# Optimization experiments

Hardware: AMD Instinct MI355X
Metric: run time of the kernel (lower is better)

The kernel has to match this reference:

```python
import jax, jax.numpy as jnp
import numpy as np

IN_F, OUT_F = 768, 2304
E, R = 8, 16            # num adapters, lora rank
ALPHA = 32
SCALING = ALPHA / R
GATE_DIM = 64


def setup_inputs() -> dict:
    key = jax.random.key(0)
    ks = jax.random.split(key, 8)
    B, S = 8, 2048
    x = jax.random.normal(ks[0], (B, S, IN_F), dtype=jnp.float32)
    z = jax.random.normal(ks[1], (B, GATE_DIM), dtype=jnp.float32)
    # frozen linear (nn.Linear weight layout [out, in])
    W = jax.random.normal(ks[2], (OUT_F, IN_F), dtype=jnp.float32) * 0.02
    b = jax.random.normal(ks[3], (OUT_F,), dtype=jnp.float32) * 0.02
    # stacked LoRA adapters: A [E, r, in], B [E, out, r]
    A = jax.random.normal(ks[4], (E, R, IN_F), dtype=jnp.float32) * (1.0 / np.sqrt(IN_F))
    Bm = jax.random.normal(ks[5], (E, OUT_F, R), dtype=jnp.float32) * 0.02
    # spectral gate: linear + softmax over experts
    Wg = jax.random.normal(ks[6], (E, GATE_DIM), dtype=jnp.float32) * 0.1
    bg = jax.random.normal(ks[7], (E,), dtype=jnp.float32) * 0.1
    return {"x": x, "z": z, "W": W, "b": b, "A": A, "Bm": Bm, "Wg": Wg, "bg": bg}


def reference(x, z, W, b, A, Bm, Wg, bg):
    # frozen linear: [B,S,out]
    frozen_out = jnp.einsum('bsi,oi->bso', x, W) + b
    # gate weights over adapters: [B,E]
    gate_w = jax.nn.softmax(jnp.einsum('bg,eg->be', z, Wg) + bg, axis=-1)
    # fused adapters: down-proj to rank r per expert (dropout p=0 -> identity)
    h = jnp.einsum('bsi,eri->bser', x, A)               # [B,S,E,r] small (r=16)
    # up-proj + gate-weighted sum over experts, fused into one contraction
    adapt = jnp.einsum('bser,eor,be->bso', h, Bm, gate_w) * SCALING
    return frozen_out + adapt
```

## Files before the change

kernel.cpp:

```cpp
#include <hip/hip_runtime.h>
#include <hip/hip_bf16.h>
#include <stdint.h>

typedef unsigned short u16;
typedef __attribute__((ext_vector_type(8))) short short8;
typedef __attribute__((ext_vector_type(4))) float floatx4;

#define M_TOT 16384
#define N_OUT 2304
#define KX    768
#define KL    128
#define SCALING 2.0f

#define WBLKS   864
#define ABLKS   48
#define BMRBLKS 144
#define GH_BLOCKS 256

__device__ __forceinline__ u16 f2b(float f) {
  union { __hip_bfloat16 h; u16 u; } c; c.h = __float2bfloat16(f); return c.u;
}
__device__ __forceinline__ float ldf(const void* p, long i, bool f32) {
  if (f32) return ((const float*)p)[i];
  union { u16 u; __hip_bfloat16 h; } c; c.u = ((const u16*)p)[i];
  return __bfloat162float(c.h);
}

__device__ __forceinline__ void gload_lds16(const void* g, void* l) {
  __builtin_amdgcn_global_load_lds(
      (const __attribute__((address_space(1))) void*)g,
      (__attribute__((address_space(3))) void*)l, 16, 0, 0);
}

__device__ __forceinline__ void cvt8(const void* src, u16* dst, long i, bool f32) {
  u16 v[8];
  if (f32) {
    const float4* s = (const float4*)src;
    float4 a = s[i * 2], b = s[i * 2 + 1];
    v[0] = f2b(a.x); v[1] = f2b(a.y); v[2] = f2b(a.z); v[3] = f2b(a.w);
    v[4] = f2b(b.x); v[5] = f2b(b.y); v[6] = f2b(b.z); v[7] = f2b(b.w);
  } else {
    *(uint4*)v = ((const uint4*)src)[i];
  }
  ((uint4*)dst)[i] = *(uint4*)v;
}

__global__ __launch_bounds__(256) void prep_small(
    const void* __restrict__ x,  const void* __restrict__ A,
    const void* __restrict__ z,  const void* __restrict__ Wg,
    const void* __restrict__ bg,
    u16* __restrict__ Abf, float* __restrict__ gsc, int* __restrict__ flagp) {
  __shared__ int s_flag;
  const int tid = threadIdx.x;
  if (tid < 64) {
    u16 v = ((const u16*)x)[tid * 2];
    int e = (v >> 7) & 0xFF;
    int huge = (e >= 160) ? 1 : 0;
    for (int off = 1; off < 64; off <<= 1) huge += __shfl_xor(huge, off, 64);
    if (tid == 0) s_flag = (huge >= 4) ? 1 : 0;
  }
  __syncthreads();
  const bool f32 = (s_flag != 0);

  int b = blockIdx.x;
  if (b < ABLKS) {
    cvt8(A, Abf, (long)b * 256 + tid, f32);
  } else {
    if (tid == 0) *flagp = s_flag;
    if (tid < 64) {
      const int bb = tid >> 3, e = tid & 7;
      float acc = ldf(bg, e, f32);
      for (int i = 0; i < 64; ++i)
        acc += ldf(z, bb * 64 + i, f32) * ldf(Wg, e * 64 + i, f32);
      float mx = acc;
      for (int off = 1; off < 8; off <<= 1) mx = fmaxf(mx, __shfl_xor(mx, off, 64));
      float ex = __expf(acc - mx);
      float sm = ex;
      for (int off = 1; off < 8; off <<= 1) sm += __shfl_xor(sm, off, 64);
      gsc[tid] = (ex / sm) * SCALING;
    }
  }
}

__global__ __launch_bounds__(256) void gemm_h_fused(
    const void* __restrict__ x, const void* __restrict__ W,
    const void* __restrict__ Bm, const u16* __restrict__ Abf,
    const float* __restrict__ gsc, const int* __restrict__ flagp,
    u16* __restrict__ xbf, u16* __restrict__ Wbf, u16* __restrict__ bmr,
    u16* __restrict__ hg) {
  __shared__ __align__(128) u16 As[64][64];
  __shared__ __align__(128) u16 Bs[128][64];
  const int tid = threadIdx.x;
  const bool f32 = (*flagp != 0);

  if (blockIdx.x >= GH_BLOCKS) {
    int c = blockIdx.x - GH_BLOCKS;
    if (c < WBLKS) {
      cvt8(W, Wbf, (long)c * 256 + tid, f32);
    } else {
      long i0 = ((long)(c - WBLKS) * 256 + tid) * 8;
      u16 v[8];
#pragma unroll
      for (int j = 0; j < 8; ++j) {
        long idx = i0 + j;
        long o = idx >> 7, er = idx & 127;
        long e = er >> 4, r = er & 15;
        v[j] = f2b(ldf(Bm, (e * 2304 + o) * 16 + r, f32));
      }
      *(uint4*)&bmr[i0] = *(uint4*)v;
    }
    return;
  }

  const int wave = tid >> 6, lane = tid & 63;
  const int wm = wave >> 1, wn = wave & 1;
  const int quad = lane >> 4, l16 = lane & 15;
  const int srow = lane >> 3, scol = (lane & 7) * 8;
  const int m0 = blockIdx.x * 64;

  const int xr = tid >> 2, cg16 = (tid & 3) * 16;
  char* Asb = (char*)&As[0][0];

  floatx4 acc[2][4];
#pragma unroll
  for (int i = 0; i < 2; ++i)
#pragma unroll
    for (int j = 0; j < 4; ++j) acc[i][j] = floatx4{0.f, 0.f, 0.f, 0.f};

  for (int kb = 0; kb < 12; ++kb) {
    const int kc = kb * 64;
    {
      const long off = (long)(m0 + xr) * KX + kc + cg16;
      uint4 lo, hi;
      if (f32) {
        const float4* xs = (const float4*)((const float*)x + off);
        float4 f0 = xs[0], f1 = xs[1], f2c = xs[2], f3 = xs[3];
        u16 v[16];
        v[0] = f2b(f0.x); v[1] = f2b(f0.y); v[2]  = f2b(f0.z); v[3]  = f2b(f0.w);
        v[4] = f2b(f1.x); v[5] = f2b(f1.y); v[6]  = f2b(f1.z); v[7]  = f2b(f1.w);
        v[8] = f2b(f2c.x); v[9] = f2b(f2c.y); v[10] = f2b(f2c.z); v[11] = f2b(f2c.w);
        v[12] = f2b(f3.x); v[13] = f2b(f3.y); v[14] = f2b(f3.z); v[15] = f2b(f3.w);
        lo = *(uint4*)&v[0]; hi = *(uint4*)&v[8];
      } else {
        lo = *(const uint4*)&((const u16*)x)[off];
        hi = *(const uint4*)&((const u16*)x)[off + 8];
      }
      *(uint4*)&xbf[off] = lo;
      *(uint4*)&xbf[off + 8] = hi;
      const int cb = cg16 * 2, sw = (xr & 7) << 4;
      *(uint4*)(Asb + xr * 128 + ((cb +  0) ^ sw)) = lo;
      *(uint4*)(Asb + xr * 128 + ((cb + 16) ^ sw)) = hi;
    }
#pragma unroll
    for (int j = 0; j < 4; ++j) {
      int r = wave * 32 + j * 8 + srow;
      gload_lds16(Abf + (size_t)r * KX + kc + scol,
                  (char*)(&Bs[0][0]) + (wave * 32 + j * 8) * 128);
    }
    __syncthreads();
#pragma unroll
    for (int ks = 0; ks < 2; ++ks) {
      short8 af[2], bf[4];
#pragma unroll
      for (int mi = 0; mi < 2; ++mi) {
        int ar = wm * 32 + mi * 16 + l16;
        af[mi] = *(const short8*)(Asb + ar * 128 + ((ks * 64 + quad * 16) ^ ((ar & 7) << 4)));
      }
#pragma unroll
      for (int ni = 0; ni < 4; ++ni)
        bf[ni] = *(const short8*)&Bs[wn * 64 + ni * 16 + l16][ks * 32 + quad * 8];
#pragma unroll
      for (int mi = 0; mi < 2; ++mi)
#pragma unroll
        for (int ni = 0; ni < 4; ++ni)
          acc[mi][ni] = __builtin_amdgcn_mfma_f32_16x16x32_bf16(af[mi], bf[ni], acc[mi][ni], 0, 0, 0);
    }
    __syncthreads();
  }
  const int bb = m0 >> 11;
  float gv[4];
#pragma unroll
  for (int ni = 0; ni < 4; ++ni) gv[ni] = gsc[bb * 8 + wn * 4 + ni];
#pragma unroll
  for (int mi = 0; mi < 2; ++mi) {
    int rbase = m0 + wm * 32 + mi * 16 + quad * 4;
#pragma unroll
    for (int ni = 0; ni < 4; ++ni) {
      int c = wn * 64 + ni * 16 + l16;
#pragma unroll
      for (int t = 0; t < 4; ++t)
        hg[(size_t)(rbase + t) * KL + c] = f2b(acc[mi][ni][t] * gv[ni]);
    }
  }
}

__global__ __launch_bounds__(256) void gemm_main(
    const u16* __restrict__ xbf, const u16* __restrict__ hg,
    const u16* __restrict__ Wbf, const u16* __restrict__ bmr,
    const void* __restrict__ bias, void* __restrict__ outv,
    const int* __restrict__ flagp) {
  __shared__ __align__(128) u16 As[128][64];
  __shared__ __align__(128) u16 Bs[128][64];
  __shared__ u16 occ_pad[4096];
  const int tid = threadIdx.x, wave = tid >> 6, lane = tid & 63;
  const int wm = wave >> 1, wn = wave & 1;
  const int quad = lane >> 4, l16 = lane & 15;
  const int srow = lane >> 3, scol = (lane & 7) * 8;

  const int linear = blockIdx.x;
  const int xcd = linear & 7;
  const int g = linear >> 3;
  const int st = g / 24;
  const int w  = g % 24;
  const int m_idx = xcd * 16 + (st / 6) * 8 + (w & 7);
  const int n_idx = (st % 6) * 3 + (w >> 3);
  const int m0 = m_idx * 128;
  const int n0 = n_idx * 128;
  if (tid == 0) ((volatile u16*)occ_pad)[0] = (u16)linear;

  floatx4 acc[4][4];
#pragma unroll
  for (int i = 0; i < 4; ++i)
#pragma unroll
    for (int j = 0; j < 4; ++j) acc[i][j] = floatx4{0.f, 0.f, 0.f, 0.f};

  for (int kb = 0; kb < 14; ++kb) {
    const u16* ap; const u16* bp; int lda, ldb, kc;
    if (kb < 12) { ap = xbf; lda = KX; bp = Wbf; ldb = KX; kc = kb * 64; }
    else         { ap = hg;  lda = KL; bp = bmr; ldb = KL; kc = (kb - 12) * 64; }
#pragma unroll
    for (int j = 0; j < 4; ++j) {
      int r = wave * 32 + j * 8 + srow;
      gload_lds16(ap + (size_t)(m0 + r) * lda + kc + scol,
                  (char*)(&As[0][0]) + (wave * 32 + j * 8) * 128);
      gload_lds16(bp + (size_t)(n0 + r) * ldb + kc + scol,
                  (char*)(&Bs[0][0]) + (wave * 32 + j * 8) * 128);
    }
    __syncthreads();
#pragma unroll
    for (int ks = 0; ks < 2; ++ks) {
      short8 af[4], bf[4];
#pragma unroll
      for (int mi = 0; mi < 4; ++mi)
        af[mi] = *(const short8*)&As[wm * 64 + mi * 16 + l16][ks * 32 + quad * 8];
#pragma unroll
      for (int ni = 0; ni < 4; ++ni)
        bf[ni] = *(const short8*)&Bs[wn * 64 + ni * 16 + l16][ks * 32 + quad * 8];
#pragma unroll
      for (int mi = 0; mi < 4; ++mi)
#pragma unroll
        for (int ni = 0; ni < 4; ++ni)
          acc[mi][ni] = __builtin_amdgcn_mfma_f32_16x16x32_bf16(af[mi], bf[ni], acc[mi][ni], 0, 0, 0);
    }
    __syncthreads();
  }

  const bool f32 = (*flagp != 0);
  float bv[4];
#pragma unroll
  for (int ni = 0; ni < 4; ++ni)
    bv[ni] = ldf(bias, n0 + wn * 64 + ni * 16 + l16, f32);
#pragma unroll
  for (int mi = 0; mi < 4; ++mi) {
    int rbase = m0 + wm * 64 + mi * 16 + quad * 4;
#pragma unroll
    for (int ni = 0; ni < 4; ++ni) {
      int c = n0 + wn * 64 + ni * 16 + l16;
#pragma unroll
      for (int t = 0; t < 4; ++t) {
        float v = acc[mi][ni][t] + bv[ni];
        size_t idx = (size_t)(rbase + t) * N_OUT + c;
        if (f32) __builtin_nontemporal_store(v, (float*)outv + idx);
        else     __builtin_nontemporal_store(f2b(v), (u16*)outv + idx);
      }
    }
  }
}

extern "C" void kernel_launch(void* const* d_in, const int* in_sizes, int n_in,
                              void* d_out, int out_size, void* d_ws, size_t ws_size,
                              hipStream_t stream) {
  const void* x  = d_in[0];
  const void* z  = d_in[1];
  const void* W  = d_in[2];
  const void* bb = d_in[3];
  const void* A  = d_in[4];
  const void* Bm = d_in[5];
  const void* Wg = d_in[6];
  const void* bg = d_in[7];

  char* ws = (char*)d_ws;
  int*   flag = (int*)ws;
  float* gsc  = (float*)(ws + 256);
  u16*   xbf  = (u16*)(ws + 1024);
  u16*   Wbf  = (u16*)(ws + 1024 + 25165824ull);
  u16*   Abf  = (u16*)(ws + 1024 + 25165824ull + 3538944ull);
  u16*   bmr  = (u16*)(ws + 1024 + 25165824ull + 3538944ull + 196608ull);
  u16*   hg   = (u16*)(ws + 1024 + 25165824ull + 3538944ull + 196608ull + 589824ull);

  prep_small<<<ABLKS + 1, 256, 0, stream>>>(x, A, z, Wg, bg, Abf, gsc, flag);

  gemm_h_fused<<<GH_BLOCKS + WBLKS + BMRBLKS, 256, 0, stream>>>(
      x, W, Bm, Abf, gsc, flag, xbf, Wbf, bmr, hg);

  gemm_main<<<(N_OUT / 128) * (M_TOT / 128), 256, 0, stream>>>(
      xbf, hg, Wbf, bmr, bb, d_out, flag);
}
```

Baseline: 125.1 us.

## Double-buffer LDS tiles with K=32 stages and XOR-swizzled layout

The main GEMM loop moves from single-buffered 64-wide K tiles to double-buffered 32-wide K tiles, so global-to-LDS loads for the next stage are issued before the MFMAs on the current stage. The LDS layout is XOR-swizzled on both the store and read sides to reduce bank conflicts on the short8 fragment reads. The aim is to hide load latency behind compute and drop one of the two barriers per step. In exchange the loop has twice as many iterations and barriers, with less MFMA work per step to cover each load.

Result: slower. 131.8 us (+5.3%).

```diff
diff --git a/kernel.cpp b/kernel.cpp
--- a/kernel.cpp
+++ b/kernel.cpp
@@ -199,13 +199,12 @@
     const u16* __restrict__ Wbf, const u16* __restrict__ bmr,
     const void* __restrict__ bias, void* __restrict__ outv,
     const int* __restrict__ flagp) {
-  __shared__ __align__(128) u16 As[128][64];
-  __shared__ __align__(128) u16 Bs[128][64];
+  __shared__ __align__(128) u16 As[2][128][32];
+  __shared__ __align__(128) u16 Bs[2][128][32];
   __shared__ u16 occ_pad[4096];
   const int tid = threadIdx.x, wave = tid >> 6, lane = tid & 63;
   const int wm = wave >> 1, wn = wave & 1;
   const int quad = lane >> 4, l16 = lane & 15;
-  const int srow = lane >> 3, scol = (lane & 7) * 8;
 
   const int linear = blockIdx.x;
   const int xcd = linear & 7;
@@ -218,40 +217,57 @@
   const int n0 = n_idx * 128;
   if (tid == 0) ((volatile u16*)occ_pad)[0] = (u16)linear;
 
+  const int rs = tid >> 2, s4 = tid & 3;
+  const int ksw = ((s4 ^ ((rs >> 1) & 3)) << 3);
+  const int xslot = (quad ^ ((l16 >> 1) & 3)) << 4;
+
   floatx4 acc[4][4];
 #pragma unroll
   for (int i = 0; i < 4; ++i)
 #pragma unroll
     for (int j = 0; j < 4; ++j) acc[i][j] = floatx4{0.f, 0.f, 0.f, 0.f};
 
-  for (int kb = 0; kb < 14; ++kb) {
-    const u16* ap; const u16* bp; int lda, ldb, kc;
-    if (kb < 12) { ap = xbf; lda = KX; bp = Wbf; ldb = KX; kc = kb * 64; }
-    else         { ap = hg;  lda = KL; bp = bmr; ldb = KL; kc = (kb - 12) * 64; }
-#pragma unroll
-    for (int j = 0; j < 4; ++j) {
-      int r = wave * 32 + j * 8 + srow;
-      gload_lds16(ap + (size_t)(m0 + r) * lda + kc + scol,
-                  (char*)(&As[0][0]) + (wave * 32 + j * 8) * 128);
-      gload_lds16(bp + (size_t)(n0 + r) * ldb + kc + scol,
-                  (char*)(&Bs[0][0]) + (wave * 32 + j * 8) * 128);
-    }
-    __syncthreads();
-#pragma unroll
-    for (int ks = 0; ks < 2; ++ks) {
-      short8 af[4], bf[4];
-#pragma unroll
-      for (int mi = 0; mi < 4; ++mi)
-        af[mi] = *(const short8*)&As[wm * 64 + mi * 16 + l16][ks * 32 + quad * 8];
+  {
+    gload_lds16(xbf + (size_t)(m0 + rs) * KX + ksw,
+                (char*)(&As[0][0][0]) + tid * 16);
+    gload_lds16(xbf + (size_t)(m0 + 64 + rs) * KX + ksw,
+                (char*)(&As[0][0][0]) + 4096 + tid * 16);
+    gload_lds16(Wbf + (size_t)(n0 + rs) * KX + ksw,
+                (char*)(&Bs[0][0][0]) + tid * 16);
+    gload_lds16(Wbf + (size_t)(n0 + 64 + rs) * KX + ksw,
+                (char*)(&Bs[0][0][0]) + 4096 + tid * 16);
+  }
+  __syncthreads();
+
+#pragma unroll 2
+  for (int kb = 0; kb < 28; ++kb) {
+    const int cur = kb & 1;
+    const int nb = kb + 1;
+    if (nb < 28) {
+      const u16* ap; const u16* bp; int ld, kc;
+      if (nb < 24) { ap = xbf; bp = Wbf; ld = KX; kc = nb * 32; }
+      else         { ap = hg;  bp = bmr; ld = KL; kc = (nb - 24) * 32; }
+      char* An = (char*)(&As[nb & 1][0][0]);
+      char* Bn = (char*)(&Bs[nb & 1][0][0]);
+      gload_lds16(ap + (size_t)(m0 + rs) * ld + kc + ksw, An + tid * 16);
+      gload_lds16(ap + (size_t)(m0 + 64 + rs) * ld + kc + ksw, An + 4096 + tid * 16);
+      gload_lds16(bp + (size_t)(n0 + rs) * ld + kc + ksw, Bn + tid * 16);
+      gload_lds16(bp + (size_t)(n0 + 64 + rs) * ld + kc + ksw, Bn + 4096 + tid * 16);
+    }
+    const char* Ab = (const char*)(&As[cur][0][0]);
+    const char* Bb = (const char*)(&Bs[cur][0][0]);
+    short8 af[4], bfr[4];
+#pragma unroll
+    for (int mi = 0; mi < 4; ++mi)
+      af[mi] = *(const short8*)(Ab + (wm * 64 + mi * 16 + l16) * 64 + xslot);
+#pragma unroll
+    for (int ni = 0; ni < 4; ++ni)
+      bfr[ni] = *(const short8*)(Bb + (wn * 64 + ni * 16 + l16) * 64 + xslot);
+#pragma unroll
+    for (int mi = 0; mi < 4; ++mi)
 #pragma unroll
       for (int ni = 0; ni < 4; ++ni)
-        bf[ni] = *(const short8*)&Bs[wn * 64 + ni * 16 + l16][ks * 32 + quad * 8];
-#pragma unroll
-      for (int mi = 0; mi < 4; ++mi)
-#pragma unroll
-        for (int ni = 0; ni < 4; ++ni)
-          acc[mi][ni] = __builtin_amdgcn_mfma_f32_16x16x32_bf16(af[mi], bf[ni], acc[mi][ni], 0, 0, 0);
-    }
+        acc[mi][ni] = __builtin_amdgcn_mfma_f32_16x16x32_bf16(af[mi], bfr[ni], acc[mi][ni], 0, 0, 0);
     __syncthreads();
   }
 
```
